# Kernel tuning notes

Measured on AMD Instinct MI355X. Metric: run time of the kernel, lower is better.

## Reference

```python
import jax, jax.numpy as jnp
import numpy as np

B, S, D, H = 4, 1024, 1024, 16
HD = D // H          # head space dim = 64
FF = 4 * D           # ffn hidden = 4096
EPS = 1e-6

# ---- Lorentz manifold helpers (curvature k=1: -t^2 + |s|^2 = -1) ----

def to_manifold(space):
    t = jnp.sqrt(jnp.sum(space * space, -1, keepdims=True) + 1.0)
    return jnp.concatenate([t, space], -1)

def l_inner(x, y):
    return -x[..., 0] * y[..., 0] + jnp.sum(x[..., 1:] * y[..., 1:], -1)

def project(z):
    # renormalize onto hyperboloid: z / sqrt(|<z,z>_L|)   (Lorentz midpoint / LResNet)
    d = jnp.sqrt(jnp.clip(-l_inner(z, z), EPS))
    return z / d[..., None]

def hyp_layernorm(x, g, b):
    s = x[..., 1:]
    mu = jnp.mean(s, -1, keepdims=True)
    var = jnp.var(s, -1, keepdims=True)
    s = (s - mu) * jax.lax.rsqrt(var + 1e-5) * g + b
    return to_manifold(s)

def apply_rope(xs, cos, sin):
    # xs [B,S,H,HD]; cos/sin [S,HD//2]; freqs broadcast as [1,S,1,HD//2]
    x2 = xs.reshape(*xs.shape[:-1], HD // 2, 2)
    c = cos[None, :, None, :]
    s = sin[None, :, None, :]
    xr = x2[..., 0] * c - x2[..., 1] * s
    xi = x2[..., 0] * s + x2[..., 1] * c
    return jnp.stack([xr, xi], -1).reshape(xs.shape)


def setup_inputs() -> dict:
    key = jax.random.key(0)
    ks = jax.random.split(key, 8)
    def w(k, shape, fan_in):
        return jax.random.normal(k, shape, jnp.float32) / np.sqrt(fan_in).astype(np.float32)
    x = to_manifold(0.5 * jax.random.normal(ks[0], (B, S, D), jnp.float32))
    pos = jnp.arange(S, dtype=jnp.float32)[:, None]
    inv = 1.0 / (10000.0 ** (jnp.arange(0, HD, 2, dtype=jnp.float32) / HD))
    ang = pos * inv[None, :]
    return {
        'x': x,
        'rope_cos': jnp.cos(ang), 'rope_sin': jnp.sin(ang),
        'norm1_g': jnp.ones((D,), jnp.float32), 'norm1_b': jnp.zeros((D,), jnp.float32),
        'Wq': w(ks[1], (H, D + 1, HD), D + 1), 'bq': jnp.zeros((H, HD), jnp.float32),
        'Wk': w(ks[2], (H, D + 1, HD), D + 1), 'bk': jnp.zeros((H, HD), jnp.float32),
        'Wv': w(ks[3], (H, D + 1, HD), D + 1), 'bv': jnp.zeros((H, HD), jnp.float32),
        'attn_scale': jnp.asarray(np.sqrt(HD), jnp.float32),
        'attn_bias': jnp.zeros((), jnp.float32),
        'Wo': w(ks[4], (H * (HD + 1), D), H * (HD + 1)), 'bo': jnp.zeros((D,), jnp.float32),
        'w_res1': jnp.asarray(1.0, jnp.float32),
        'norm2_g': jnp.ones((D,), jnp.float32), 'norm2_b': jnp.zeros((D,), jnp.float32),
        'W1': w(ks[5], (D + 1, FF), D + 1), 'b1': jnp.zeros((FF,), jnp.float32),
        'W2': w(ks[6], (FF + 1, D), FF + 1), 'b2': jnp.zeros((D,), jnp.float32),
        'w_res2': jnp.asarray(1.0, jnp.float32),
    }


def reference(x, rope_cos, rope_sin, norm1_g, norm1_b, Wq, bq, Wk, bk, Wv, bv,
              attn_scale, attn_bias, Wo, bo, w_res1, norm2_g, norm2_b,
              W1, b1, W2, b2, w_res2):
    # ---- pre-norm ----
    xn = hyp_layernorm(x, norm1_g, norm1_b)
    # ---- per-head Lorentz linear (space part), inline RoPE on q/k ----
    qs = jnp.einsum('bsd,hde->bshe', xn, Wq) + bq          # [B,S,H,HD]
    ksp = jnp.einsum('bsd,hde->bshe', xn, Wk) + bk
    vsp = jnp.einsum('bsd,hde->bshe', xn, Wv) + bv
    qs = apply_rope(qs, rope_cos, rope_sin)
    ksp = apply_rope(ksp, rope_cos, rope_sin)
    # hyperbolic normalization of q/k: unit space norm, time recomputed
    qs = qs * jax.lax.rsqrt(jnp.sum(qs * qs, -1, keepdims=True) + EPS)
    ksp = ksp * jax.lax.rsqrt(jnp.sum(ksp * ksp, -1, keepdims=True) + EPS)
    q = to_manifold(qs)                                    # [B,S,H,HD+1]
    k = to_manifold(ksp)
    v = to_manifold(vsp)
    # ---- curvature-aware scores: 2 + 2 <q,k>_L (neg sq Lorentz distance) ----
    sgn = jnp.concatenate([-jnp.ones((1,), q.dtype), jnp.ones((HD,), q.dtype)])
    cin = jnp.einsum('bshe,bthe->bhst', q * sgn, k)        # Minkowski inner [B,H,S,S]
    att = (2.0 + 2.0 * cin) / attn_scale + attn_bias
    P = jax.nn.softmax(att, axis=-1)
    # ---- Lorentz midpoint aggregation of values ----
    m = jnp.einsum('bhst,bthe->bshe', P, v)
    m = project(m)                                         # back onto hyperboloid
    # ---- heads concat + output Lorentz linear ----
    cat = m.reshape(B, S, H * (HD + 1))
    attn_out = to_manifold(cat @ Wo + bo)
    # ---- LResNet residual 1 ----
    x = project(x + w_res1 * attn_out)
    # ---- Lorentz FFN ----
    h = hyp_layernorm(x, norm2_g, norm2_b)
    h = to_manifold(jax.nn.gelu(h @ W1 + b1))
    mlp = to_manifold(h @ W2 + b2)
    # ---- LResNet residual 2 ----
    x = project(x + w_res2 * mlp)
    return x
```

## Files before the change

### kernel.cpp

```cpp
#include <hip/hip_runtime.h>
#include <hip/hip_bf16.h>

typedef __hip_bfloat16 bf16;
typedef __attribute__((ext_vector_type(8))) short short8;
typedef __attribute__((ext_vector_type(4))) float f32x4;

#define B_  4
#define S_  1024
#define H_  16
#define R_  4096

#define MBL 1048576L
#define OFF_WQKVT (0L)
#define OFF_X2    (0L)
#define OFF_WOT   (6L*MBL + MBL/2)
#define OFF_W1T   (9L*MBL)
#define OFF_W2T   (17L*MBL + MBL/2)
#define OFF_BIAS  (26L*MBL)
#define OFF_XNB   (27L*MBL)
#define OFF_MCAT  (27L*MBL)
#define OFF_MLP   (27L*MBL)
#define OFF_QPS   (36L*MBL)
#define OFF_ARAW  (36L*MBL)
#define OFF_QT    (44L*MBL)
#define OFF_KPS   (45L*MBL)
#define OFF_HBUF  (45L*MBL)
#define OFF_KT    (53L*MBL)
#define OFF_VT    (54L*MBL)
#define OFF_HHC   (54L*MBL)
#define OFF_HHBIG (54L*MBL)
#define BQKV 0
#define BOF  16384
#define B1F  32768
#define B2F  65536
#define W2R0 81920
#define RCF  98304
#define RSNF 262144
#define SCLF 409600
#define TACC 425984
#define FLAG 458752

__device__ __forceinline__ bf16  f2bf(float v) { return __float2bfloat16(v); }
__device__ __forceinline__ float bf2f(bf16 v)  { return __bfloat162float(v); }
__device__ __forceinline__ unsigned short bf2s(float v) {
  return __builtin_bit_cast(unsigned short, __float2bfloat16(v));
}
__device__ __forceinline__ float ldu(const void* p, long i, int isbf) {
  return isbf ? bf2f(((const bf16*)p)[i]) : ((const float*)p)[i];
}
__device__ __forceinline__ void stu(void* p, long i, float v, int isbf) {
  if (isbf) ((bf16*)p)[i] = f2bf(v);
  else      ((float*)p)[i] = v;
}

__device__ __forceinline__ void gload16(const bf16* g, short* l) {
  __builtin_amdgcn_global_load_lds(
      (const __attribute__((address_space(1))) unsigned int*)g,
      (__attribute__((address_space(3))) unsigned int*)l, 16, 0, 0);
}

__global__ void detect_kernel(const unsigned* __restrict__ g, int* __restrict__ flag) {
  if (threadIdx.x == 0) flag[0] = (g[0] == 0x3F803F80u) ? 1 : 0;
}

__global__ __launch_bounds__(256) void zero16_kernel(uint4* __restrict__ p, int n16) {
  int i = blockIdx.x * 256 + threadIdx.x;
  if (i < n16) p[i] = uint4{0, 0, 0, 0};
}

__global__ __launch_bounds__(256) void prep_misc(
    const void* bq, const void* bk, const void* bv, const void* bo, const void* b1,
    const void* b2, const void* W2, const void* rc, const void* rsn,
    const void* scl, const void* ab, const void* wr1, const void* wr2,
    char* bias_base, const int* __restrict__ flag) {
  const int isbf = flag[0];
  int i = blockIdx.x * 256 + threadIdx.x;
  float* bqkvf = (float*)(bias_base + BQKV);
  if (i < 1024)        { bqkvf[i] = ldu(bq, i, isbf); return; }
  if (i < 2048)        { bqkvf[i] = ldu(bk, i - 1024, isbf); return; }
  if (i < 3072)        { bqkvf[i] = ldu(bv, i - 2048, isbf); return; }
  if (i < 4096)        { ((float*)(bias_base + BOF))[i - 3072] = ldu(bo, i - 3072, isbf); return; }
  if (i < 8192)        { ((float*)(bias_base + B1F))[i - 4096] = ldu(b1, i - 4096, isbf); return; }
  if (i < 9216)        { ((float*)(bias_base + B2F))[i - 8192] = ldu(b2, i - 8192, isbf); return; }
  if (i < 10240)       { ((float*)(bias_base + W2R0))[i - 9216] = ldu(W2, i - 9216, isbf); return; }
  if (i < 10240+32768) { ((float*)(bias_base + RCF))[i - 10240] = ldu(rc, i - 10240, isbf); return; }
  if (i < 10240+65536) { ((float*)(bias_base + RSNF))[i - 43008] = ldu(rsn, i - 43008, isbf); return; }
  if (i == 75776)      { ((float*)(bias_base + SCLF))[0] = ldu(scl, 0, isbf); return; }
  if (i == 75777)      { ((float*)(bias_base + SCLF))[1] = ldu(ab, 0, isbf); return; }
  if (i == 75778)      { ((float*)(bias_base + SCLF))[2] = ldu(wr1, 0, isbf); return; }
  if (i == 75779)      { ((float*)(bias_base + SCLF))[3] = ldu(wr2, 0, isbf); return; }
}

__global__ __launch_bounds__(256) void transp_gen(const void* __restrict__ src, long src_off,
                                                  int src_rows, int src_ld,
                                                  bf16* __restrict__ dst, int dst_ld,
                                                  const int* __restrict__ flag) {
  const int isbf = flag[0];
  __shared__ float tl[64][65];
  int t = threadIdx.x, tx = t & 63, tg = t >> 6;
  int k0 = blockIdx.x * 64, n0 = blockIdx.y * 64;
  for (int i = tg; i < 64; i += 4) {
    int k = k0 + i;
    tl[i][tx] = (k < src_rows) ? ldu(src, src_off + (long)k * src_ld + n0 + tx, isbf) : 0.f;
  }
  __syncthreads();
  for (int i = tg; i < 64; i += 4) {
    int k = k0 + tx;
    if (k < dst_ld) dst[(long)(n0 + i) * dst_ld + k] = f2bf(tl[tx][i]);
  }
}

__global__ __launch_bounds__(256) void transp_qkv(const void* __restrict__ Wq,
                                                  const void* __restrict__ Wk,
                                                  const void* __restrict__ Wv,
                                                  bf16* __restrict__ dst,
                                                  const int* __restrict__ flag) {
  const int isbf = flag[0];
  __shared__ float tl[64][65];
  int t = threadIdx.x, tx = t & 63, tg = t >> 6;
  int k0 = blockIdx.x * 64;
  int z = blockIdx.y, mode = z >> 4, h = z & 15;
  const void* src = (mode == 0) ? Wq : (mode == 1) ? Wk : Wv;
  const long soff = (long)h * 1025 * 64;
  int base_n = mode * 1024 + h * 64;
  for (int i = tg; i < 64; i += 4) {
    int k = k0 + i;
    tl[i][tx] = (k < 1025) ? ldu(src, soff + (long)k * 64 + tx, isbf) : 0.f;
  }
  __syncthreads();
  for (int i = tg; i < 64; i += 4) {
    int k = k0 + tx;
    if (k < 1056) dst[(long)(base_n + i) * 1056 + k] = f2bf(tl[tx][i]);
  }
}

__global__ __launch_bounds__(256) void transp_wo(const void* __restrict__ src,
                                                 bf16* __restrict__ dst,
                                                 const int* __restrict__ flag) {
  const int isbf = flag[0];
  __shared__ float tl[64][65];
  int t = threadIdx.x, tx = t & 63, tg = t >> 6;
  int k0 = blockIdx.x * 64, n0 = blockIdx.y * 64;
  for (int i = tg; i < 64; i += 4) {
    int kp = k0 + i;
    int h = kp / 66, e = kp - h * 66;
    float v = 0.f;
    if (kp < 1056 && e < 65) v = ldu(src, (long)(h * 65 + e) * 1024 + n0 + tx, isbf);
    tl[i][tx] = v;
  }
  __syncthreads();
  for (int i = tg; i < 64; i += 4) {
    int kp = k0 + tx;
    if (kp < 1056) dst[(long)(n0 + i) * 1056 + kp] = f2bf(tl[tx][i]);
  }
}

__device__ __forceinline__ float bred_f(float v, float* sh) {
#pragma unroll
  for (int o = 32; o; o >>= 1) v += __shfl_xor(v, o);
  __syncthreads();
  if ((threadIdx.x & 63) == 0) sh[threadIdx.x >> 6] = v;
  __syncthreads();
  return sh[0] + sh[1] + sh[2] + sh[3];
}
__device__ __forceinline__ double bred_d(double v, double* sh) {
#pragma unroll
  for (int o = 32; o; o >>= 1) v += __shfl_xor(v, o);
  __syncthreads();
  if ((threadIdx.x & 63) == 0) sh[threadIdx.x >> 6] = v;
  __syncthreads();
  return sh[0] + sh[1] + sh[2] + sh[3];
}

__global__ __launch_bounds__(256) void ln_kernel(const void* __restrict__ x, int xtag,
                                                 const void* __restrict__ g,
                                                 const void* __restrict__ b,
                                                 bf16* __restrict__ out,
                                                 const int* __restrict__ flag) {
  const int isbf = flag[0];
  const int xb = (xtag == 2) ? isbf : xtag;
  __shared__ float red[4];
  const long base = (long)blockIdx.x * 1025;
  const long obase = (long)blockIdx.x * 1056;
  const int tid = threadIdx.x;
  float v[4];
#pragma unroll
  for (int i = 0; i < 4; i++) v[i] = ldu(x, base + 1 + tid * 4 + i, xb);
  float s = 0.f, s2 = 0.f;
#pragma unroll
  for (int i = 0; i < 4; i++) { s += v[i]; s2 += v[i] * v[i]; }
  s  = bred_f(s,  red);
  s2 = bred_f(s2, red);
  const float mu  = s * (1.f / 1024.f);
  const float var = s2 * (1.f / 1024.f) - mu * mu;
  const float rs  = rsqrtf(var + 1e-5f);
  float n[4], ns = 0.f;
#pragma unroll
  for (int i = 0; i < 4; i++) {
    const int e = tid * 4 + i;
    n[i] = (v[i] - mu) * rs * ldu(g, e, isbf) + ldu(b, e, isbf);
    ns += n[i] * n[i];
  }
  ns = bred_f(ns, red);
  if (tid == 0) out[obase] = f2bf(sqrtf(ns + 1.f));
#pragma unroll
  for (int i = 0; i < 4; i++) out[obase + 1 + tid * 4 + i] = f2bf(n[i]);
  if (tid < 31) out[obase + 1025 + tid] = f2bf(0.f);
}

template <int EPI, bool SS>
__global__ __launch_bounds__(256) void mfma_gemm(const bf16* __restrict__ A, int lda,
                                                 const bf16* __restrict__ Bw, int ldb, int K,
                                                 const float* __restrict__ bias,
                                                 void* __restrict__ Cv, int ldc, int accf,
                                                 float* __restrict__ tacc) {
  __shared__ __align__(16) short As[128 * 32];
  __shared__ __align__(16) short Bs[64 * 32];
  const int tid = threadIdx.x, lane = tid & 63, wv = tid >> 6;
  const int quad = lane >> 4, q15 = lane & 15;
  const int wave_m = wv & 1, wave_n = wv >> 1;
  const int n0 = blockIdx.x * 64, m0 = blockIdx.y * 128;
  const int sa0 = wv * 128 + lane, sa1 = sa0 + 64;
  const int ra0 = sa0 >> 2, ca0 = (sa0 & 3) ^ (ra0 & 3);
  const int ra1 = sa1 >> 2, ca1 = (sa1 & 3) ^ (ra1 & 3);
  const int rb = tid >> 2, cb = (tid & 3) ^ (rb & 3);
  const int kswz = (quad ^ (q15 & 3)) * 8;
  f32x4 acc[4][2] = {};
  for (int k0 = 0; k0 < K; k0 += 32) {
    gload16(A + (long)(m0 + ra0) * lda + k0 + ca0 * 8, As + sa0 * 8);
    gload16(A + (long)(m0 + ra1) * lda + k0 + ca1 * 8, As + sa1 * 8);
    gload16(Bw + (long)(n0 + rb) * ldb + k0 + cb * 8, Bs + tid * 8);
    __syncthreads();
    short8 af[4], bfr[2];
#pragma unroll
    for (int i = 0; i < 4; i++)
      af[i] = *(const short8*)(As + (wave_m * 64 + i * 16 + q15) * 32 + kswz);
#pragma unroll
    for (int i = 0; i < 2; i++)
      bfr[i] = *(const short8*)(Bs + (wave_n * 32 + i * 16 + q15) * 32 + kswz);
#pragma unroll
    for (int mi = 0; mi < 4; mi++)
#pragma unroll
      for (int ni = 0; ni < 2; ni++)
        acc[mi][ni] = __builtin_amdgcn_mfma_f32_16x16x32_bf16(af[mi], bfr[ni], acc[mi][ni], 0, 0, 0);
    __syncthreads();
  }
#pragma unroll
  for (int mi = 0; mi < 4; mi++) {
#pragma unroll
    for (int r = 0; r < 4; r++) {
      const int m = m0 + wave_m * 64 + mi * 16 + quad * 4 + r;
      float s2 = 0.f;
#pragma unroll
      for (int ni = 0; ni < 2; ni++) {
        const int n = n0 + wave_n * 32 + ni * 16 + q15;
        float v = acc[mi][ni][r] + (bias ? bias[n] : 0.f);
        const long idx = (long)m * ldc + n;
        if (EPI == 0) {
          float* Cf = (float*)Cv;
          if (accf) v += Cf[idx];
          Cf[idx] = v;
        } else if (EPI == 1) {
          ((bf16*)Cv)[idx] = f2bf(v);
        } else {
          const float t = tanhf(0.7978845608028654f * (v + 0.044715f * v * v * v));
          v = 0.5f * v * (1.f + t);
          ((bf16*)Cv)[idx] = f2bf(v);
        }
        if (SS) s2 += v * v;
      }
      if (SS) {
        s2 += __shfl_xor(s2, 1);
        s2 += __shfl_xor(s2, 2);
        s2 += __shfl_xor(s2, 4);
        s2 += __shfl_xor(s2, 8);
        if (q15 == 0) atomicAdd(tacc + m, s2);
      }
    }
  }
}

__global__ __launch_bounds__(256) void gemm_qkv(const bf16* __restrict__ A,
                                                const bf16* __restrict__ Wt,
                                                const char* __restrict__ bias_base,
                                                bf16* __restrict__ qPs, float* __restrict__ qtc,
                                                bf16* __restrict__ kPs, float* __restrict__ ktc,
                                                bf16* __restrict__ vT) {
  __shared__ __align__(16) short As[128 * 32];
  __shared__ __align__(16) short Bs[128 * 32];
  const int tid = threadIdx.x, lane = tid & 63, wv = tid >> 6;
  const int quad = lane >> 4, q15 = lane & 15;
  const int wave_m = wv & 1, wave_n = wv >> 1;
  const int n0 = blockIdx.x * 128, m0 = blockIdx.y * 128;
  const int s0 = wv * 128 + lane, s1 = s0 + 64;
  const int r0 = s0 >> 2, c0 = (s0 & 3) ^ (r0 & 3);
  const int r1 = s1 >> 2, c1 = (s1 & 3) ^ (r1 & 3);
  const int kswz = (quad ^ (q15 & 3)) * 8;
  const float* bqkvf = (const float*)(bias_base + BQKV);
  const float* rcf   = (const float*)(bias_base + RCF);
  const float* rsnf  = (const float*)(bias_base + RSNF);
  f32x4 acc[4][4] = {};
  for (int k0 = 0; k0 < 1056; k0 += 32) {
    gload16(A + (long)(m0 + r0) * 1056 + k0 + c0 * 8, As + s0 * 8);
    gload16(A + (long)(m0 + r1) * 1056 + k0 + c1 * 8, As + s1 * 8);
    gload16(Wt + (long)(n0 + r0) * 1056 + k0 + c0 * 8, Bs + s0 * 8);
    gload16(Wt + (long)(n0 + r1) * 1056 + k0 + c1 * 8, Bs + s1 * 8);
    __syncthreads();
    short8 af[4], bfr[4];
#pragma unroll
    for (int i = 0; i < 4; i++) {
      af[i]  = *(const short8*)(As + (wave_m * 64 + i * 16 + q15) * 32 + kswz);
      bfr[i] = *(const short8*)(Bs + (wave_n * 64 + i * 16 + q15) * 32 + kswz);
    }
#pragma unroll
    for (int mi = 0; mi < 4; mi++)
#pragma unroll
      for (int ni = 0; ni < 4; ni++)
        acc[mi][ni] = __builtin_amdgcn_mfma_f32_16x16x32_bf16(af[mi], bfr[ni], acc[mi][ni], 0, 0, 0);
    __syncthreads();
  }
  const int hg = (n0 >> 6) + wave_n;
  const int mode = hg >> 4, h = hg & 15;
  const int nb = hg * 64;
#pragma unroll
  for (int mi = 0; mi < 4; mi++) {
#pragma unroll
    for (int r = 0; r < 4; r++) {
      const int m = m0 + wave_m * 64 + mi * 16 + quad * 4 + r;
      const int bb = m >> 10, s = m & 1023;
      const int bh = bb * H_ + h;
      float v[4];
#pragma unroll
      for (int ns = 0; ns < 4; ns++) v[ns] = acc[mi][ns][r] + bqkvf[nb + ns * 16 + q15];
      if (mode < 2) {
#pragma unroll
        for (int ns = 0; ns < 4; ns++) {
          const int eg = ns * 16 + q15;
          const int j = eg >> 1;
          const float c = rcf[s * 32 + j], sn = rsnf[s * 32 + j];
          const float p = __shfl_xor(v[ns], 1);
          v[ns] = ((eg & 1) == 0) ? (v[ns] * c - p * sn) : (p * sn + v[ns] * c);
        }
      }
      float ss = v[0] * v[0] + v[1] * v[1] + v[2] * v[2] + v[3] * v[3];
#pragma unroll
      for (int o = 8; o; o >>= 1) ss += __shfl_xor(ss, o);
      if (mode == 0) {
        const float sc = rsqrtf(ss + 1e-6f);
        const long rb = (long)(bh * 1024 + s) * 64;
#pragma unroll
        for (int ns = 0; ns < 4; ns++) qPs[rb + ns * 16 + q15] = f2bf(v[ns] * sc);
        if (q15 == 0) qtc[bh * 1024 + s] = sqrtf(ss / (ss + 1e-6f) + 1.f);
      } else if (mode == 1) {
        const float sc = rsqrtf(ss + 1e-6f);
        const long rb = (long)(bh * 1024 + s) * 64;
#pragma unroll
        for (int ns = 0; ns < 4; ns++) kPs[rb + ns * 16 + q15] = f2bf(v[ns] * sc);
        if (q15 == 0) ktc[bh * 1024 + s] = sqrtf(ss / (ss + 1e-6f) + 1.f);
      } else {
        const long vb = (long)bh * 81920;
#pragma unroll
        for (int ns = 0; ns < 4; ns++) vT[vb + (long)(1 + ns * 16 + q15) * 1024 + s] = f2bf(v[ns]);
        if (q15 == 0) vT[vb + s] = f2bf(sqrtf(ss + 1.f));
      }
    }
  }
}

__global__ __launch_bounds__(256) void attn_kernel(const bf16* __restrict__ qPs,
                                                   const float* __restrict__ qtc,
                                                   const bf16* __restrict__ kPs,
                                                   const float* __restrict__ ktc,
                                                   const bf16* __restrict__ vT,
                                                   const float* __restrict__ scalf,
                                                   bf16* __restrict__ mcat) {
  __shared__ __align__(16) short kbuf[64 * 72];
  __shared__ __align__(16) short vbuf[80 * 72];
  __shared__ __align__(16) short pbuf[64 * 72];
  __shared__ float tkl[64];
  const int tid = threadIdx.x, lane = tid & 63, wv = tid >> 6;
  const int quad = lane >> 4, q15 = lane & 15;
  const int id = blockIdx.x;
  const int cxd = id & 7, jj_ = id >> 3;
  const int bh = cxd * 8 + (jj_ & 7), qt_ = jj_ >> 3;
  const float inv_scale = 1.f / scalf[0];
  const long qrow = (long)(bh * 1024 + qt_ * 64 + wv * 16 + q15) * 64;
  const short8 aq0 = *(const short8*)(qPs + qrow + quad * 8);
  const short8 aq1 = *(const short8*)(qPs + qrow + 32 + quad * 8);
  float tqr[4];
#pragma unroll
  for (int r = 0; r < 4; r++) tqr[r] = qtc[bh * 1024 + qt_ * 64 + wv * 16 + quad * 4 + r];
  f32x4 out[5];
#pragma unroll
  for (int mt = 0; mt < 5; mt++) out[mt] = f32x4{0, 0, 0, 0};
  float lip[4] = {0.f, 0.f, 0.f, 0.f};
  const int srcl = (q15 >> 2) << 4;
  for (int kt = 0; kt < 16; kt++) {
    __syncthreads();
#pragma unroll
    for (int c = 0; c < 2; c++) {
      const int id2 = c * 256 + tid, row = id2 >> 3, off = id2 & 7;
      *(uint4*)(kbuf + row * 72 + off * 8) =
          *(const uint4*)(kPs + (long)(bh * 1024 + kt * 64 + row) * 64 + off * 8);
    }
#pragma unroll
    for (int c = 0; c < 3; c++) {
      const int id2 = c * 256 + tid;
      if (id2 < 640) {
        const int row = id2 >> 3, off = id2 & 7;
        *(uint4*)(vbuf + row * 72 + off * 8) =
            *(const uint4*)(vT + (long)bh * 81920 + (long)row * 1024 + kt * 64 + off * 8);
      }
    }
    if (tid < 64) tkl[tid] = ktc[bh * 1024 + kt * 64 + tid];
    __syncthreads();
    f32x4 sacc[4] = {f32x4{0,0,0,0}, f32x4{0,0,0,0}, f32x4{0,0,0,0}, f32x4{0,0,0,0}};
#pragma unroll
    for (int ns = 0; ns < 4; ns++) {
      short8 b0 = *(const short8*)(kbuf + (ns * 16 + q15) * 72 + quad * 8);
      short8 b1 = *(const short8*)(kbuf + (ns * 16 + q15) * 72 + 32 + quad * 8);
      sacc[ns] = __builtin_amdgcn_mfma_f32_16x16x32_bf16(aq0, b0, sacc[ns], 0, 0, 0);
      sacc[ns] = __builtin_amdgcn_mfma_f32_16x16x32_bf16(aq1, b1, sacc[ns], 0, 0, 0);
    }
#pragma unroll
    for (int ns = 0; ns < 4; ns++) {
      const float tk = tkl[ns * 16 + q15];
#pragma unroll
      for (int r = 0; r < 4; r++) {
        const float pv = __expf((2.f + 2.f * (sacc[ns][r] - tqr[r] * tk)) * inv_scale);
        lip[r] += pv;
        pbuf[(wv * 16 + quad * 4 + r) * 72 + ns * 16 + q15] = (short)bf2s(pv);
      }
    }
#pragma unroll
    for (int mt = 0; mt < 5; mt++)
#pragma unroll
      for (int kc = 0; kc < 2; kc++) {
        short8 av = *(const short8*)(vbuf + (mt * 16 + q15) * 72 + kc * 32 + quad * 8);
        short8 bp = *(const short8*)(pbuf + (wv * 16 + q15) * 72 + kc * 32 + quad * 8);
        out[mt] = __builtin_amdgcn_mfma_f32_16x16x32_bf16(av, bp, out[mt], 0, 0, 0);
      }
  }
  {
#pragma unroll
    for (int o = 8; o; o >>= 1)
#pragma unroll
      for (int r = 0; r < 4; r++) lip[r] += __shfl_xor(lip[r], o);
    float linv[4];
#pragma unroll
    for (int r = 0; r < 4; r++) linv[r] = 1.f / lip[r];
    const float t0 = __shfl(linv[0], srcl), t1 = __shfl(linv[1], srcl);
    const float t2 = __shfl(linv[2], srcl), t3 = __shfl(linv[3], srcl);
    const int rr = q15 & 3;
    const float lv = (rr == 0) ? t0 : (rr == 1) ? t1 : (rr == 2) ? t2 : t3;
#pragma unroll
    for (int mt = 0; mt < 5; mt++)
#pragma unroll
      for (int j = 0; j < 4; j++) out[mt][j] *= lv;
  }
  float part = 0.f;
#pragma unroll
  for (int mt = 0; mt < 5; mt++)
#pragma unroll
    for (int j = 0; j < 4; j++) {
      const int e = mt * 16 + quad * 4 + j;
      const float vv = out[mt][j] * out[mt][j];
      part += (e == 0) ? vv : -vv;
    }
  part += __shfl_xor(part, 16);
  part += __shfl_xor(part, 32);
  const float dinv = rsqrtf(fmaxf(part, 1e-6f));
  __syncthreads();
  short* obuf = vbuf;
  const int qrow_l = wv * 16 + q15;
#pragma unroll
  for (int mt = 0; mt < 5; mt++)
#pragma unroll
    for (int j = 0; j < 4; j++) {
      const int e = mt * 16 + quad * 4 + j;
      if (e <= 64) obuf[qrow_l * 72 + e] = (short)bf2s(out[mt][j] * dinv);
    }
  if (quad == 1) obuf[qrow_l * 72 + 65] = 0;
  __syncthreads();
  const int b = bh >> 4, h = bh & 15;
  const long outbase = ((long)b * 1024 + qt_ * 64) * 1056 + h * 66;
  for (int i = tid; i < 64 * 33; i += 256) {
    const int row = i / 33, p = i - row * 33;
    *(unsigned*)(mcat + outbase + (long)row * 1056 + p * 2) =
        *(const unsigned*)(obuf + row * 72 + p * 2);
  }
}

__global__ __launch_bounds__(256) void final_fix_kernel(const float* __restrict__ t_acc,
                                                        const float* __restrict__ w2r0,
                                                        const float* __restrict__ b2f,
                                                        float* __restrict__ mlp) {
  const int m = blockIdx.x;
  const float t = sqrtf(1.f + t_acc[m]);
  float* row = mlp + (long)m * 1024;
  for (int n = threadIdx.x; n < 1024; n += 256) row[n] += t * w2r0[n] + b2f[n];
}

__global__ __launch_bounds__(256) void res_project_kernel(
    const void* __restrict__ x, int xtag, const void* __restrict__ c, int ctag,
    const float* __restrict__ scalf, int widx, void* __restrict__ out, int otag,
    const int* __restrict__ flag) {
  const int isbf = flag[0];
  const int xb = (xtag == 2) ? isbf : xtag;
  const int cb2 = (ctag == 2) ? isbf : ctag;
  const int ob = (otag == 2) ? isbf : otag;
  __shared__ double red[4];
  const long bx = (long)blockIdx.x * 1025;
  const long bc = (long)blockIdx.x * 1024;
  const int tid = threadIdx.x;
  const double w = (double)scalf[widx];
  const float x0 = ldu(x, bx, xb);
  float xs[4], cv[4];
#pragma unroll
  for (int i = 0; i < 4; i++) {
    xs[i] = ldu(x, bx + 1 + tid * 4 + i, xb);
    cv[i] = ldu(c, bc + tid * 4 + i, cb2);
  }
  double cc = 0.0, xx = 0.0, xc = 0.0;
#pragma unroll
  for (int i = 0; i < 4; i++) {
    cc += (double)cv[i] * cv[i];
    xx += (double)xs[i] * xs[i];
    xc += (double)xs[i] * cv[i];
  }
  cc = bred_d(cc, red);
  xx = bred_d(xx, red);
  xc = bred_d(xc, red);
  const double t   = sqrt(1.0 + cc);
  const double lxx = (double)x0 * x0 - xx;
  const double xm  = -(double)x0 * t + xc;
  double d2 = lxx + w * w - 2.0 * w * xm;
  if (d2 < 1e-6) d2 = 1e-6;
  const double dinv = 1.0 / sqrt(d2);
  if (tid == 0) stu(out, bx, (float)(((double)x0 + w * t) * dinv), ob);
#pragma unroll
  for (int i = 0; i < 4; i++)
    stu(out, bx + 1 + tid * 4 + i, (float)(((double)xs[i] + w * cv[i]) * dinv), ob);
}

extern "C" void kernel_launch(void* const* d_in, const int* in_sizes, int n_in,
                              void* d_out, int out_size, void* d_ws, size_t ws_size,
                              hipStream_t stream) {
  char* w = (char*)d_ws;
  char* bias_base = w + OFF_BIAS;
  int* flag = (int*)(bias_base + FLAG);
  float* tacc = (float*)(bias_base + TACC);
  const float* scalf = (const float*)(bias_base + SCLF);
  const bool big = ws_size >= (size_t)92 * MBL;

  detect_kernel<<<1, 64, 0, stream>>>((const unsigned*)d_in[3], flag);
  zero16_kernel<<<4, 256, 0, stream>>>((uint4*)tacc, 1024);

  prep_misc<<<297, 256, 0, stream>>>(
      d_in[6], d_in[8], d_in[10], d_in[14], d_in[19], d_in[21], d_in[20], d_in[1],
      d_in[2], d_in[11], d_in[12], d_in[15], d_in[22], bias_base, flag);
  transp_qkv<<<dim3(17, 48), 256, 0, stream>>>(d_in[5], d_in[7], d_in[9],
                                               (bf16*)(w + OFF_WQKVT), flag);
  transp_wo<<<dim3(17, 16), 256, 0, stream>>>(d_in[13], (bf16*)(w + OFF_WOT), flag);
  transp_gen<<<dim3(17, 64), 256, 0, stream>>>(d_in[18], 0, 1025, 4096,
                                               (bf16*)(w + OFF_W1T), 1056, flag);
  transp_gen<<<dim3(64, 16), 256, 0, stream>>>(d_in[20], 1024, 4096, 1024,
                                               (bf16*)(w + OFF_W2T), 4096, flag);
  ln_kernel<<<R_, 256, 0, stream>>>(d_in[0], 2, d_in[3], d_in[4], (bf16*)(w + OFF_XNB), flag);

  gemm_qkv<<<dim3(24, 32), 256, 0, stream>>>(
      (const bf16*)(w + OFF_XNB), (const bf16*)(w + OFF_WQKVT), bias_base,
      (bf16*)(w + OFF_QPS), (float*)(w + OFF_QT), (bf16*)(w + OFF_KPS),
      (float*)(w + OFF_KT), (bf16*)(w + OFF_VT));
  attn_kernel<<<1024, 256, 0, stream>>>(
      (const bf16*)(w + OFF_QPS), (const float*)(w + OFF_QT), (const bf16*)(w + OFF_KPS),
      (const float*)(w + OFF_KT), (const bf16*)(w + OFF_VT), scalf, (bf16*)(w + OFF_MCAT));
  mfma_gemm<1, false><<<dim3(16, 32), 256, 0, stream>>>(
      (const bf16*)(w + OFF_MCAT), 1056, (const bf16*)(w + OFF_WOT), 1056, 1056,
      (const float*)(bias_base + BOF), w + OFF_ARAW, 1024, 0, nullptr);
  res_project_kernel<<<R_, 256, 0, stream>>>(d_in[0], 2, w + OFF_ARAW, 1, scalf, 2,
                                             w + OFF_X2, 1, flag);
  ln_kernel<<<R_, 256, 0, stream>>>(w + OFF_X2, 1, d_in[16], d_in[17],
                                    (bf16*)(w + OFF_HBUF), flag);
  if (big) {
    mfma_gemm<2, true><<<dim3(64, 32), 256, 0, stream>>>(
        (const bf16*)(w + OFF_HBUF), 1056, (const bf16*)(w + OFF_W1T), 1056, 1056,
        (const float*)(bias_base + B1F), w + OFF_HHBIG, 4096, 0, tacc);
    mfma_gemm<0, false><<<dim3(16, 32), 256, 0, stream>>>(
        (const bf16*)(w + OFF_HHBIG), 4096, (const bf16*)(w + OFF_W2T), 4096, 4096,
        nullptr, w + OFF_MLP, 1024, 0, nullptr);
  } else {
    for (int c = 0; c < 4; c++) {
      mfma_gemm<2, true><<<dim3(16, 32), 256, 0, stream>>>(
          (const bf16*)(w + OFF_HBUF), 1056, (const bf16*)(w + OFF_W1T) + (long)c * 1024 * 1056,
          1056, 1056, (const float*)(bias_base + B1F) + c * 1024, w + OFF_HHC, 1024, 0, tacc);
      mfma_gemm<0, false><<<dim3(16, 32), 256, 0, stream>>>(
          (const bf16*)(w + OFF_HHC), 1024, (const bf16*)(w + OFF_W2T) + c * 1024, 4096, 1024,
          nullptr, w + OFF_MLP, 1024, c > 0 ? 1 : 0, nullptr);
    }
  }
  final_fix_kernel<<<R_, 256, 0, stream>>>(tacc, (const float*)(bias_base + W2R0),
                                           (const float*)(bias_base + B2F),
                                           (float*)(w + OFF_MLP));
  res_project_kernel<<<R_, 256, 0, stream>>>(w + OFF_X2, 1, w + OFF_MLP, 0, scalf, 3,
                                             d_out, 2, flag);
}
```

Before: 547.7 us.

## Use 128x128 tile GEMM for FFN up-projection and cheaper exp-based GELU

Adds a new MFMA GEMM kernel with a 128x128 output tile (4x4 MFMA fragments per wave) and uses it for the W1 GEMM with fused GELU and sum-of-squares epilogue. The larger tile doubles reuse of the A and B fragments loaded from LDS, cutting global and LDS traffic per FLOP compared with the 128x64 tile. GELU's tanhf is replaced by an __expf-based tanh formula to shorten the epilogue. The new kernel has no double buffering and holds more accumulator registers, which may lower occupancy.

```diff
diff --git a/kernel.cpp b/kernel.cpp
--- a/kernel.cpp
+++ b/kernel.cpp
@@ -52,6 +52,11 @@
   if (isbf) ((bf16*)p)[i] = f2bf(v);
   else      ((float*)p)[i] = v;
 }
+__device__ __forceinline__ float gelu_f(float v) {
+  const float u = 0.7978845608028654f * (v + 0.044715f * v * v * v);
+  const float e = __expf(fminf(2.f * u, 80.f));
+  return 0.5f * v * (1.f + (e - 1.f) / (e + 1.f));
+}
 
 __device__ __forceinline__ void gload16(const bf16* g, short* l) {
   __builtin_amdgcn_global_load_lds(
@@ -263,8 +268,77 @@
         } else if (EPI == 1) {
           ((bf16*)Cv)[idx] = f2bf(v);
         } else {
-          const float t = tanhf(0.7978845608028654f * (v + 0.044715f * v * v * v));
-          v = 0.5f * v * (1.f + t);
+          v = gelu_f(v);
+          ((bf16*)Cv)[idx] = f2bf(v);
+        }
+        if (SS) s2 += v * v;
+      }
+      if (SS) {
+        s2 += __shfl_xor(s2, 1);
+        s2 += __shfl_xor(s2, 2);
+        s2 += __shfl_xor(s2, 4);
+        s2 += __shfl_xor(s2, 8);
+        if (q15 == 0) atomicAdd(tacc + m, s2);
+      }
+    }
+  }
+}
+
+template <int EPI, bool SS>
+__global__ __launch_bounds__(256) void mfma_gemm128(const bf16* __restrict__ A, int lda,
+                                                    const bf16* __restrict__ Bw, int ldb, int K,
+                                                    const float* __restrict__ bias,
+                                                    void* __restrict__ Cv, int ldc, int accf,
+                                                    float* __restrict__ tacc) {
+  __shared__ __align__(16) short As[128 * 32];
+  __shared__ __align__(16) short Bs[128 * 32];
+  const int tid = threadIdx.x, lane = tid & 63, wv = tid >> 6;
+  const int quad = lane >> 4, q15 = lane & 15;
+  const int wave_m = wv & 1, wave_n = wv >> 1;
+  const int n0 = blockIdx.x * 128, m0 = blockIdx.y * 128;
+  const int s0 = wv * 128 + lane, s1 = s0 + 64;
+  const int r0 = s0 >> 2, c0 = (s0 & 3) ^ (r0 & 3);
+  const int r1 = s1 >> 2, c1 = (s1 & 3) ^ (r1 & 3);
+  const int kswz = (quad ^ (q15 & 3)) * 8;
+  f32x4 acc[4][4] = {};
+  for (int k0 = 0; k0 < K; k0 += 32) {
+    gload16(A + (long)(m0 + r0) * lda + k0 + c0 * 8, As + s0 * 8);
+    gload16(A + (long)(m0 + r1) * lda + k0 + c1 * 8, As + s1 * 8);
+    gload16(Bw + (long)(n0 + r0) * ldb + k0 + c0 * 8, Bs + s0 * 8);
+    gload16(Bw + (long)(n0 + r1) * ldb + k0 + c1 * 8, Bs + s1 * 8);
+    __syncthreads();
+    short8 af[4], bfr[4];
+#pragma unroll
+    for (int i = 0; i < 4; i++) {
+      af[i]  = *(const short8*)(As + (wave_m * 64 + i * 16 + q15) * 32 + kswz);
+      bfr[i] = *(const short8*)(Bs + (wave_n * 64 + i * 16 + q15) * 32 + kswz);
+    }
+#pragma unroll
+    for (int mi = 0; mi < 4; mi++)
+#pragma unroll
+      for (int ni = 0; ni < 4; ni++)
+        acc[mi][ni] = __builtin_amdgcn_mfma_f32_16x16x32_bf16(af[mi], bfr[ni], acc[mi][ni], 0, 0, 0);
+    __syncthreads();
+  }
+#pragma unroll
+  for (int mi = 0; mi < 4; mi++) {
+#pragma unroll
+    for (int r = 0; r < 4; r++) {
+      const int m = m0 + wave_m * 64 + mi * 16 + quad * 4 + r;
+      float s2 = 0.f;
+#pragma unroll
+      for (int ni = 0; ni < 4; ni++) {
+        const int n = n0 + wave_n * 64 + ni * 16 + q15;
+        float v = acc[mi][ni][r] + (bias ? bias[n] : 0.f);
+        const long idx = (long)m * ldc + n;
+        if (EPI == 0) {
+          float* Cf = (float*)Cv;
+          if (accf) v += Cf[idx];
+          Cf[idx] = v;
+        } else if (EPI == 1) {
+          ((bf16*)Cv)[idx] = f2bf(v);
+        } else {
+          v = gelu_f(v);
           ((bf16*)Cv)[idx] = f2bf(v);
         }
         if (SS) s2 += v * v;
@@ -583,7 +657,7 @@
   ln_kernel<<<R_, 256, 0, stream>>>(w + OFF_X2, 1, d_in[16], d_in[17],
                                     (bf16*)(w + OFF_HBUF), flag);
   if (big) {
-    mfma_gemm<2, true><<<dim3(64, 32), 256, 0, stream>>>(
+    mfma_gemm128<2, true><<<dim3(32, 32), 256, 0, stream>>>(
         (const bf16*)(w + OFF_HBUF), 1056, (const bf16*)(w + OFF_W1T), 1056, 1056,
         (const float*)(bias_base + B1F), w + OFF_HHBIG, 4096, 0, tacc);
     mfma_gemm<0, false><<<dim3(16, 32), 256, 0, stream>>>(
```

Result: no change. 546.5 us (-0.2%).
